# Kernel tuning notes

Hardware: AMD Instinct MI355X
Metric: run time of the kernel (lower is better)

The kernel has to match this reference:

```python
import jax, jax.numpy as jnp
import numpy as np
from jax import lax

# --- quadrature config for K_nu(x) = exp(-x) * int_0^inf exp(-x*(cosh t - 1)) * cosh(nu*t) dt ---
# Integrand is even and analytic; trapezoid on [0, T_MAX] converges spectrally.
_T_MAX = 6.0
_N_QUAD = 192


def _bessel_k(x, nu):
    """Modified Bessel K_nu(x) for x > 0 via integral-representation quadrature.

    Replaces the torch module's host round-trip to scipy.special.kv with an
    on-device, jit- and autodiff-compatible evaluation. exp(x) is factored out
    for stability at large x.
    """
    t = jnp.linspace(0.0, _T_MAX, _N_QUAD, dtype=x.dtype)
    h = t[1] - t[0]
    w = jnp.full((_N_QUAD,), h, dtype=x.dtype).at[0].mul(0.5).at[-1].mul(0.5)
    cosh_t = jnp.cosh(t)              # [Q]
    cosh_nut = jnp.cosh(nu * t)       # [Q]

    def step(acc, tw):
        ct, chnt, wk = tw
        return acc + (wk * chnt) * jnp.exp(-x * (ct - 1.0)), None

    integral, _ = lax.scan(step, jnp.zeros_like(x), (cosh_t, cosh_nut, w))
    return jnp.exp(-x) * integral


def _matern_general(dist, nu, var, lengthscale):
    # scaled = sqrt(2*nu) * r / l, clamped like the torch code
    scaled = jnp.maximum(jnp.sqrt(2.0 * nu) * dist / lengthscale, 1e-10)
    log_norm = (1.0 - nu) * jnp.log(2.0) - lax.lgamma(nu)
    k = var * jnp.exp(log_norm) * jnp.power(scaled, nu) * _bessel_k(scaled, nu)
    # square kernel matrix: diagonal is exactly var (masked_fill in torch)
    n = k.shape[0]
    eye = jnp.eye(n, dtype=bool)
    return jnp.where(eye, var, k)


def setup_inputs() -> dict:
    key = jax.random.key(0)
    k1, = jax.random.split(key, 1)
    X1 = jax.random.normal(k1, (1024, 32), dtype=jnp.float32)
    # learned scalar parameters (learn_nu / learn_variance / learn_lengthscale = True)
    nu = jnp.asarray(12.73, dtype=jnp.float32)
    log_variance = jnp.asarray(np.log(1.5), dtype=jnp.float32)
    log_lengthscale = jnp.asarray(np.log(2.0), dtype=jnp.float32)
    return {"X1": X1, "nu": nu, "log_variance": log_variance, "log_lengthscale": log_lengthscale}


def reference(X1, nu, log_variance, log_lengthscale):
    var = jnp.exp(log_variance)
    lengthscale = jnp.exp(log_lengthscale)
    # pairwise Euclidean distances (cdist, p=2); eps floor kills inf grad at r=0
    sq_norms = jnp.sum(X1 * X1, axis=1)
    sq = sq_norms[:, None] + sq_norms[None, :] - 2.0 * (X1 @ X1.T)   # [N, N]
    dist = jnp.sqrt(jnp.maximum(sq, 1e-24))
    return _matern_general(dist, nu, var, lengthscale)
```

## Files before the change

### kernel.cpp

```cpp
#include <hip/hip_runtime.h>
#include <math.h>

#define NQ 192
#define TMAX 6.0f
#define LOG2E 1.44269504088896340736f
#define LN2   0.69314718055994530942f

__global__ __launch_bounds__(192) void matern_coef_kernel(
    const float* __restrict__ nu_p, const float* __restrict__ lv_p,
    const float* __restrict__ ll_p, float2* __restrict__ coef,
    float* __restrict__ scal)
{
    const int t = threadIdx.x;
    const float nu = nu_p[0];
    const float h = TMAX / (float)(NQ - 1);
    const float tq = h * (float)t;
    const float w  = (t == 0 || t == NQ - 1) ? 0.5f * h : h;
    const float cosh_t  = 0.5f * (__expf(tq) + __expf(-tq));
    const float cosh_nt = 0.5f * (__expf(nu * tq) + __expf(-nu * tq));
    coef[t] = make_float2(cosh_t * LOG2E, w * cosh_nt);
    if (t == 0) {
        const float var = __expf(lv_p[0]);
        const float ls  = __expf(ll_p[0]);
        scal[0] = sqrtf(2.0f * nu) / ls;
        scal[1] = var * __expf((1.0f - nu) * LN2 - lgammaf(nu));
        scal[2] = var;
        scal[3] = nu;
    }
}

__global__ __launch_bounds__(64) void matern_tri_kernel(
    const float* __restrict__ X,
    const float4* __restrict__ coef4,
    const float* __restrict__ scal,
    float* __restrict__ out, int N)
{
    __shared__ float sXi[16][36];
    __shared__ float sXj[16][36];
    __shared__ float sT[16][17];
    __shared__ float4 sC4[NQ / 2];

    const int lane = threadIdx.x;
    const int nt = N >> 4;

    int rem = (int)blockIdx.x, by = 0;
    while (rem >= nt - by) { rem -= nt - by; ++by; }
    const int bx = by + rem;
    const int i0 = by << 4, j0 = bx << 4;

    #pragma unroll
    for (int u = 0; u < 2; ++u) {
        int f = lane + (u << 6);
        int r = f >> 3, c4 = (f & 7) << 2;
        *(float4*)&sXi[r][c4] = *(const float4*)&X[(i0 + r) * 32 + c4];
        *(float4*)&sXj[r][c4] = *(const float4*)&X[(j0 + r) * 32 + c4];
    }
    for (int u = lane; u < NQ / 2; u += 64) sC4[u] = coef4[u];
    __syncthreads();

    const float scale = scal[0], norm = scal[1], var = scal[2], nu = scal[3];

    const int jl = lane & 15;
    const int i4 = (lane >> 4) << 2;

    float d2[4] = {0.f, 0.f, 0.f, 0.f};
    #pragma unroll
    for (int d = 0; d < 32; ++d) {
        const float xj = sXj[jl][d];
        #pragma unroll
        for (int k = 0; k < 4; ++k) {
            const float df = sXi[i4 + k][d] - xj;
            d2[k] = fmaf(df, df, d2[k]);
        }
    }

    float x[4], xn[4], acc[4];
    #pragma unroll
    for (int k = 0; k < 4; ++k) {
        const float dist = sqrtf(fmaxf(d2[k], 1e-24f));
        x[k]  = fmaxf(scale * dist, 1e-10f);
        xn[k] = -x[k];
        acc[k] = 0.f;
    }

    float xmin = fminf(fminf(x[0], x[1]), fminf(x[2], x[3]));
    #pragma unroll
    for (int o = 32; o > 0; o >>= 1) xmin = fminf(xmin, __shfl_xor(xmin, o));
    const float cosh_cut = 150.0f / (LOG2E * xmin);
    int qp = NQ / 2;
    if (cosh_cut < 205.0f) {
        const float y = cosh_cut + sqrtf(fmaxf(cosh_cut * cosh_cut - 1.0f, 0.0f));
        const float tcut = LN2 * __builtin_amdgcn_logf(fmaxf(y, 1.0f));
        const float h = TMAX / (float)(NQ - 1);
        const int idx = (int)(tcut / h) + 1;
        qp = min(NQ / 2, (idx >> 1) + 1);
    }
    qp = __builtin_amdgcn_readfirstlane(qp);

    #pragma unroll 2
    for (int q = 0; q < qp; ++q) {
        const float4 cc = sC4[q];
        #pragma unroll
        for (int k = 0; k < 4; ++k)
            acc[k] = fmaf(cc.y, __builtin_amdgcn_exp2f(xn[k] * cc.x), acc[k]);
        #pragma unroll
        for (int k = 0; k < 4; ++k)
            acc[k] = fmaf(cc.w, __builtin_amdgcn_exp2f(xn[k] * cc.z), acc[k]);
    }

    #pragma unroll
    for (int k = 0; k < 4; ++k) {
        const float pw = __builtin_amdgcn_exp2f(nu * __builtin_amdgcn_logf(x[k]));
        float val = norm * pw * acc[k];
        const int gi = i0 + i4 + k, gj = j0 + jl;
        if (gi == gj) val = var;
        out[gi * N + gj] = val;
        sT[i4 + k][jl] = val;
    }
    if (bx != by) {
        __syncthreads();
        #pragma unroll
        for (int k = 0; k < 4; ++k) {
            const int a = i4 + k;
            out[(j0 + a) * N + (i0 + jl)] = sT[jl][a];
        }
    }
}

extern "C" void kernel_launch(void* const* d_in, const int* in_sizes, int n_in,
                              void* d_out, int out_size, void* d_ws, size_t ws_size,
                              hipStream_t stream) {
    const float* X  = (const float*)d_in[0];
    const float* nu = (const float*)d_in[1];
    const float* lv = (const float*)d_in[2];
    const float* ll = (const float*)d_in[3];
    float* out = (float*)d_out;

    const int N = in_sizes[0] / 32;
    float2* coef = (float2*)d_ws;
    float*  scal = (float*)d_ws + 2 * NQ;

    matern_coef_kernel<<<1, NQ, 0, stream>>>(nu, lv, ll, coef, scal);

    const int nt = N / 16;
    const int nblk = nt * (nt + 1) / 2;
    matern_tri_kernel<<<nblk, 64, 0, stream>>>(X, (const float4*)coef, scal, out, N);
}
```

Before: 75.04 us.

## Fuse coefficient setup into tile kernel and truncate quadrature by relative tolerance

The separate single-block coefficient kernel is removed: each tile block now computes its quadrature nodes, weights and scalar constants in shared memory, which saves one launch and a global round-trip. The block becomes 128 threads computing two outputs each instead of 64 threads computing four. The triangular tile index is found with a closed-form sqrt estimate instead of a loop. The quadrature cutoff is now set per element by solving a fixed-point equation for where terms drop below a relative tolerance of the result, with the wave taking the maximum. This drops far more nodes than the old absolute exp2 underflow cutoff, but adds a small truncation error and redundant per-block coefficient work.

```diff
diff --git a/kernel.cpp b/kernel.cpp
--- a/kernel.cpp
+++ b/kernel.cpp
@@ -5,123 +5,131 @@
 #define TMAX 6.0f
 #define LOG2E 1.44269504088896340736f
 #define LN2   0.69314718055994530942f
+#define HSTEP (6.0f / 191.0f)
+#define INVH  (191.0f / 6.0f)
 
-__global__ __launch_bounds__(192) void matern_coef_kernel(
-    const float* __restrict__ nu_p, const float* __restrict__ lv_p,
-    const float* __restrict__ ll_p, float2* __restrict__ coef,
-    float* __restrict__ scal)
-{
-    const int t = threadIdx.x;
-    const float nu = nu_p[0];
-    const float h = TMAX / (float)(NQ - 1);
-    const float tq = h * (float)t;
-    const float w  = (t == 0 || t == NQ - 1) ? 0.5f * h : h;
-    const float cosh_t  = 0.5f * (__expf(tq) + __expf(-tq));
-    const float cosh_nt = 0.5f * (__expf(nu * tq) + __expf(-nu * tq));
-    coef[t] = make_float2(cosh_t * LOG2E, w * cosh_nt);
-    if (t == 0) {
-        const float var = __expf(lv_p[0]);
-        const float ls  = __expf(ll_p[0]);
-        scal[0] = sqrtf(2.0f * nu) / ls;
-        scal[1] = var * __expf((1.0f - nu) * LN2 - lgammaf(nu));
-        scal[2] = var;
-        scal[3] = nu;
-    }
+__device__ __forceinline__ float fast_ln(float v) {
+    return LN2 * __builtin_amdgcn_logf(v);
 }
 
-__global__ __launch_bounds__(64) void matern_tri_kernel(
+__global__ __launch_bounds__(128) void matern_tri_kernel(
     const float* __restrict__ X,
-    const float4* __restrict__ coef4,
-    const float* __restrict__ scal,
+    const float* __restrict__ nu_p, const float* __restrict__ lv_p,
+    const float* __restrict__ ll_p,
     float* __restrict__ out, int N)
 {
     __shared__ float sXi[16][36];
     __shared__ float sXj[16][36];
     __shared__ float sT[16][17];
-    __shared__ float4 sC4[NQ / 2];
+    __shared__ __align__(16) float4 sC4[NQ / 2];
+    __shared__ float sScal[4];
 
-    const int lane = threadIdx.x;
+    const int t  = threadIdx.x;
     const int nt = N >> 4;
+    const int tot = 2 * nt + 1;
 
-    int rem = (int)blockIdx.x, by = 0;
-    while (rem >= nt - by) { rem -= nt - by; ++by; }
-    const int bx = by + rem;
+    const int B = (int)blockIdx.x;
+    int by = (int)(((float)tot - sqrtf((float)(tot * tot - 8 * B))) * 0.5f);
+    if (by < 0) by = 0;
+    while (by * (tot - by) / 2 > B) --by;
+    while ((by + 1) * (tot - by - 1) / 2 <= B) ++by;
+    const int bx = by + (B - by * (tot - by) / 2);
     const int i0 = by << 4, j0 = bx << 4;
 
-    #pragma unroll
-    for (int u = 0; u < 2; ++u) {
-        int f = lane + (u << 6);
-        int r = f >> 3, c4 = (f & 7) << 2;
+    {
+        const int r = t >> 3, c4 = (t & 7) << 2;
         *(float4*)&sXi[r][c4] = *(const float4*)&X[(i0 + r) * 32 + c4];
         *(float4*)&sXj[r][c4] = *(const float4*)&X[(j0 + r) * 32 + c4];
     }
-    for (int u = lane; u < NQ / 2; u += 64) sC4[u] = coef4[u];
+
+    const float nu = nu_p[0];
+
+    if (t < 96) {
+        const float tq0 = HSTEP * (float)(2 * t);
+        const float tq1 = HSTEP * (float)(2 * t + 1);
+        const float w0 = (t == 0)  ? 0.5f * HSTEP : HSTEP;
+        const float w1 = (t == 95) ? 0.5f * HSTEP : HSTEP;
+        const float ch0 = 0.5f * (__expf(tq0) + __expf(-tq0));
+        const float ch1 = 0.5f * (__expf(tq1) + __expf(-tq1));
+        const float cn0 = 0.5f * (__expf(nu * tq0) + __expf(-nu * tq0));
+        const float cn1 = 0.5f * (__expf(nu * tq1) + __expf(-nu * tq1));
+        sC4[t] = make_float4(ch0 * LOG2E, w0 * cn0, ch1 * LOG2E, w1 * cn1);
+    }
+    if (t == 127) {
+        const float var = __expf(lv_p[0]);
+        const float ls  = __expf(ll_p[0]);
+        const float lnorm = fast_ln(var) + (1.0f - nu) * LN2 - lgammaf(nu);
+        sScal[0] = sqrtf(2.0f * nu) / ls;
+        sScal[1] = __expf(lnorm);
+        sScal[2] = var;
+        sScal[3] = lnorm + fast_ln(HSTEP) + 12.72f;
+    }
     __syncthreads();
 
-    const float scale = scal[0], norm = scal[1], var = scal[2], nu = scal[3];
+    const float scale = sScal[0], norm = sScal[1], var = sScal[2], Cbase = sScal[3];
 
-    const int jl = lane & 15;
-    const int i4 = (lane >> 4) << 2;
+    const int jl = t & 15;
+    const int i2 = (t >> 4) << 1;
 
-    float d2[4] = {0.f, 0.f, 0.f, 0.f};
+    float d2[2] = {0.f, 0.f};
     #pragma unroll
     for (int d = 0; d < 32; ++d) {
         const float xj = sXj[jl][d];
         #pragma unroll
-        for (int k = 0; k < 4; ++k) {
-            const float df = sXi[i4 + k][d] - xj;
+        for (int k = 0; k < 2; ++k) {
+            const float df = sXi[i2 + k][d] - xj;
             d2[k] = fmaf(df, df, d2[k]);
         }
     }
 
-    float x[4], xn[4], acc[4];
+    float x[2], xn[2], acc[2];
+    bool isdiag[2];
     #pragma unroll
-    for (int k = 0; k < 4; ++k) {
+    for (int k = 0; k < 2; ++k) {
         const float dist = sqrtf(fmaxf(d2[k], 1e-24f));
         x[k]  = fmaxf(scale * dist, 1e-10f);
         xn[k] = -x[k];
         acc[k] = 0.f;
+        isdiag[k] = (i0 + i2 + k) == (j0 + jl);
     }
 
-    float xmin = fminf(fminf(x[0], x[1]), fminf(x[2], x[3]));
+    const float xe = fminf(isdiag[0] ? 1e30f : x[0], isdiag[1] ? 1e30f : x[1]);
+    const float C  = Cbase + nu * fast_ln(xe);
+    const float rr = nu / xe;
+    float tc = fast_ln(rr + sqrtf(fmaf(rr, rr, 1.0f)));
     #pragma unroll
-    for (int o = 32; o > 0; o >>= 1) xmin = fminf(xmin, __shfl_xor(xmin, o));
-    const float cosh_cut = 150.0f / (LOG2E * xmin);
-    int qp = NQ / 2;
-    if (cosh_cut < 205.0f) {
-        const float y = cosh_cut + sqrtf(fmaxf(cosh_cut * cosh_cut - 1.0f, 0.0f));
-        const float tcut = LN2 * __builtin_amdgcn_logf(fmaxf(y, 1.0f));
-        const float h = TMAX / (float)(NQ - 1);
-        const int idx = (int)(tcut / h) + 1;
-        qp = min(NQ / 2, (idx >> 1) + 1);
+    for (int it = 0; it < 4; ++it) {
+        const float c = (C + nu * tc) / xe;
+        tc = (c > 1.0f) ? fast_ln(c + sqrtf(fmaf(c, c, -1.0f))) : 0.0f;
     }
+    tc = fminf(tc, TMAX);
+    int qp = min(NQ / 2, (int)(tc * INVH) / 2 + 3);
+    #pragma unroll
+    for (int o = 32; o > 0; o >>= 1) qp = max(qp, __shfl_xor(qp, o));
     qp = __builtin_amdgcn_readfirstlane(qp);
 
     #pragma unroll 2
     for (int q = 0; q < qp; ++q) {
         const float4 cc = sC4[q];
-        #pragma unroll
-        for (int k = 0; k < 4; ++k)
-            acc[k] = fmaf(cc.y, __builtin_amdgcn_exp2f(xn[k] * cc.x), acc[k]);
-        #pragma unroll
-        for (int k = 0; k < 4; ++k)
-            acc[k] = fmaf(cc.w, __builtin_amdgcn_exp2f(xn[k] * cc.z), acc[k]);
+        acc[0] = fmaf(cc.y, __builtin_amdgcn_exp2f(xn[0] * cc.x), acc[0]);
+        acc[1] = fmaf(cc.y, __builtin_amdgcn_exp2f(xn[1] * cc.x), acc[1]);
+        acc[0] = fmaf(cc.w, __builtin_amdgcn_exp2f(xn[0] * cc.z), acc[0]);
+        acc[1] = fmaf(cc.w, __builtin_amdgcn_exp2f(xn[1] * cc.z), acc[1]);
     }
 
     #pragma unroll
-    for (int k = 0; k < 4; ++k) {
+    for (int k = 0; k < 2; ++k) {
         const float pw = __builtin_amdgcn_exp2f(nu * __builtin_amdgcn_logf(x[k]));
         float val = norm * pw * acc[k];
-        const int gi = i0 + i4 + k, gj = j0 + jl;
-        if (gi == gj) val = var;
-        out[gi * N + gj] = val;
-        sT[i4 + k][jl] = val;
+        if (isdiag[k]) val = var;
+        out[(i0 + i2 + k) * N + (j0 + jl)] = val;
+        sT[i2 + k][jl] = val;
     }
     if (bx != by) {
         __syncthreads();
         #pragma unroll
-        for (int k = 0; k < 4; ++k) {
-            const int a = i4 + k;
+        for (int k = 0; k < 2; ++k) {
+            const int a = i2 + k;
             out[(j0 + a) * N + (i0 + jl)] = sT[jl][a];
         }
     }
@@ -136,13 +144,8 @@
     const float* ll = (const float*)d_in[3];
     float* out = (float*)d_out;
 
-    const int N = in_sizes[0] / 32;
-    float2* coef = (float2*)d_ws;
-    float*  scal = (float*)d_ws + 2 * NQ;
-
-    matern_coef_kernel<<<1, NQ, 0, stream>>>(nu, lv, ll, coef, scal);
-
+    const int N  = in_sizes[0] / 32;
     const int nt = N / 16;
     const int nblk = nt * (nt + 1) / 2;
-    matern_tri_kernel<<<nblk, 64, 0, stream>>>(X, (const float4*)coef, scal, out, N);
+    matern_tri_kernel<<<nblk, 128, 0, stream>>>(X, nu, lv, ll, out, N);
 }
```

New measurement: 67.63 us. -9.9%, faster.
